# Kernel optimization log

Measured on AMD Instinct MI355X. Metric: run time of the kernel, lower is better.

## Reference

```python
import jax, jax.numpy as jnp
import numpy as np

# PyTorch LSTM gate order: i, f, g, o. Dropout layers are identity in eval mode.

def _lstm_step(w_ih, w_hh, b):
    def step(carry, xt):
        h, c = carry
        g = xt @ w_ih.T + h @ w_hh.T + b
        i, f, gg, o = jnp.split(g, 4, axis=-1)
        c = jax.nn.sigmoid(f) * c + jax.nn.sigmoid(i) * jnp.tanh(gg)
        h = jax.nn.sigmoid(o) * jnp.tanh(c)
        return (h, c), h
    return step


def bilstm(x, wf_ih, wf_hh, bf_ih, bf_hh, wb_ih, wb_hh, bb_ih, bb_hh):
    # x: [B, T, D] -> out: [B, T, 2H]
    B = x.shape[0]
    H = wf_hh.shape[1]
    xt = jnp.swapaxes(x, 0, 1)  # [T, B, D]
    init = (jnp.zeros((B, H), x.dtype), jnp.zeros((B, H), x.dtype))
    _, hf = jax.lax.scan(_lstm_step(wf_ih, wf_hh, bf_ih + bf_hh), init, xt)
    _, hb = jax.lax.scan(_lstm_step(wb_ih, wb_hh, bb_ih + bb_hh), init, xt[::-1])
    hb = hb[::-1]
    return jnp.swapaxes(jnp.concatenate([hf, hb], axis=-1), 0, 1)


def setup_inputs() -> dict:
    key = jax.random.key(0)
    ks = iter(jax.random.split(key, 64))
    d = {"x": jax.random.normal(next(ks), (1024, 1024, 8), jnp.float32)}
    layer_dims = [(16, 20), (40, 20), (40, 10), (20, 10)]
    for li, (din, H) in enumerate(layer_dims, start=1):
        for dr in ("f", "b"):
            d[f"w{li}{dr}_ih"] = 0.1 * jax.random.normal(next(ks), (4 * H, din), jnp.float32)
            d[f"w{li}{dr}_hh"] = 0.1 * jax.random.normal(next(ks), (4 * H, H), jnp.float32)
            d[f"b{li}{dr}_ih"] = 0.1 * jax.random.normal(next(ks), (4 * H,), jnp.float32)
            d[f"b{li}{dr}_hh"] = 0.1 * jax.random.normal(next(ks), (4 * H,), jnp.float32)
    d["fc_w"] = 0.1 * jax.random.normal(next(ks), (1, 20), jnp.float32)
    d["fc_b"] = 0.1 * jax.random.normal(next(ks), (1,), jnp.float32)
    return d


def reference(x,
              w1f_ih, w1f_hh, b1f_ih, b1f_hh, w1b_ih, w1b_hh, b1b_ih, b1b_hh,
              w2f_ih, w2f_hh, b2f_ih, b2f_hh, w2b_ih, w2b_hh, b2b_ih, b2b_hh,
              w3f_ih, w3f_hh, b3f_ih, b3f_hh, w3b_ih, w3b_hh, b3b_ih, b3b_hh,
              w4f_ih, w4f_hh, b4f_ih, b4f_hh, w4b_ih, w4b_hh, b4b_ih, b4b_hh,
              fc_w, fc_b):
    # lag-1 concat: [B,T,8] -> [B,T,16]
    x_lag = jnp.concatenate([jnp.zeros_like(x[:, :1, :]), x[:, :-1, :]], axis=1)
    h = jnp.concatenate([x, x_lag], axis=2)
    h = bilstm(h, w1f_ih, w1f_hh, b1f_ih, b1f_hh, w1b_ih, w1b_hh, b1b_ih, b1b_hh)
    h = bilstm(h, w2f_ih, w2f_hh, b2f_ih, b2f_hh, w2b_ih, w2b_hh, b2b_ih, b2b_hh)
    h = bilstm(h, w3f_ih, w3f_hh, b3f_ih, b3f_hh, w3b_ih, w3b_hh, b3b_ih, b3b_hh)
    h = bilstm(h, w4f_ih, w4f_hh, b4f_ih, b4f_hh, w4b_ih, w4b_hh, b4b_ih, b4b_hh)
    h = h[:, -1, :]  # [B, 20]
    return jax.nn.sigmoid(h @ fc_w.T + fc_b)
```

## Files before the change

### kernel.cpp

```cpp
#include <hip/hip_runtime.h>
#include <hip/hip_fp16.h>
#include <stdint.h>

#define B_TOTAL 1024
#define T_TOTAL 1024
#define LOG2E 1.44269504088896f

typedef _Float16 f16x2 __attribute__((ext_vector_type(2)));

__device__ __forceinline__ float dot2acc(uint32_t xw, f16x2 w, float acc) {
#if __has_builtin(__builtin_amdgcn_fdot2)
    return __builtin_amdgcn_fdot2(__builtin_bit_cast(f16x2, xw), w, acc, false);
#else
    f16x2 xv = __builtin_bit_cast(f16x2, xw);
    return acc + (float)xv.x * (float)w.x + (float)xv.y * (float)w.y;
#endif
}

__device__ __forceinline__ uint32_t packf2(float a, float b) {
    f16x2 t;
    t.x = (_Float16)a;
    t.y = (_Float16)b;
    return __builtin_bit_cast(uint32_t, t);
}

__device__ __forceinline__ float sigm_(float z) {
    float e = __builtin_amdgcn_exp2f(-LOG2E * z);
    return __builtin_amdgcn_rcpf(1.0f + e);
}
__device__ __forceinline__ float tanh_(float z) {
    float e = __builtin_amdgcn_exp2f((2.0f * LOG2E) * z);
    float r = __builtin_amdgcn_rcpf(1.0f + e);
    return __builtin_fmaf(-2.0f, r, 1.0f);
}

__device__ __forceinline__ void wavebar() {
#if __has_builtin(__builtin_amdgcn_wave_barrier)
    __builtin_amdgcn_wave_barrier();
#endif
}

template <int DIN, int H, bool LAYER1, bool STORE_ALL>
__global__ void __launch_bounds__(64, 1) lstm_scan(
    const float* __restrict__ x,
    const __half* __restrict__ inbuf,
    const float* __restrict__ wihf, const float* __restrict__ whhf,
    const float* __restrict__ bihf, const float* __restrict__ bhhf,
    const float* __restrict__ wihb, const float* __restrict__ whhb,
    const float* __restrict__ bihb, const float* __restrict__ bhhb,
    __half* __restrict__ outbuf,
    float* __restrict__ lasth)
{
    constexpr int GPW   = 64 / H;
    constexpr int ND    = DIN / 2;
    constexpr int NH    = H / 2;
    constexpr int HS_DW = (H == 20) ? 12 : 8;

    const int dir  = blockIdx.y;
    const int lane = threadIdx.x;
    const int g    = lane / H;
    const int j    = lane - g * H;
    const int b    = blockIdx.x * GPW + g;
    const bool valid = (g < GPW) && (b < B_TOTAL);
    const int bs   = valid ? b : (B_TOTAL - 1);

    const float* w_ih = dir ? wihb : wihf;
    const float* w_hh = dir ? whhb : whhf;
    const float* b_ih = dir ? bihb : bihf;
    const float* b_hh = dir ? bhhb : bhhf;

    __shared__ uint32_t hsm[GPW + 1][HS_DW];

    f16x2 wih2[4][ND];
    f16x2 whh2[4][NH];
    float bias[4];
#pragma unroll
    for (int q = 0; q < 4; ++q) {
        const int r = q * H + j;
#pragma unroll
        for (int d = 0; d < ND; ++d) {
            f16x2 t;
            t.x = (_Float16)w_ih[r * DIN + 2 * d];
            t.y = (_Float16)w_ih[r * DIN + 2 * d + 1];
            wih2[q][d] = t;
        }
#pragma unroll
        for (int k = 0; k < NH; ++k) {
            f16x2 t;
            t.x = (_Float16)w_hh[r * H + 2 * k];
            t.y = (_Float16)w_hh[r * H + 2 * k + 1];
            whh2[q][k] = t;
        }
        bias[q] = b_ih[r] + b_hh[r];
    }

    const int tstep = dir ? -1 : 1;
    int tt = dir ? (T_TOTAL - 1) : 0;

    __half* op = nullptr;
    ptrdiff_t opstep = 0;
    if constexpr (STORE_ALL) {
        op = outbuf + (size_t)tt * (B_TOTAL * 2 * H) + (size_t)bs * (2 * H) + dir * H + j;
        opstep = (ptrdiff_t)tstep * (B_TOTAL * 2 * H);
    }

    float c = 0.0f;
    float hlast = 0.0f;
    ((__half*)&hsm[g][0])[j] = __float2half(0.0f);
    wavebar();

    auto tail = [&](const uint32_t* hd, float a0, float a1, float a2, float a3) {
#pragma unroll
        for (int k = 0; k < NH; ++k) {
            a0 = dot2acc(hd[k], whh2[0][k], a0);
            a1 = dot2acc(hd[k], whh2[1][k], a1);
            a2 = dot2acc(hd[k], whh2[2][k], a2);
            a3 = dot2acc(hd[k], whh2[3][k], a3);
        }
        const float iv = sigm_(a0);
        const float fv = sigm_(a1);
        const float gv = tanh_(a2);
        const float ov = sigm_(a3);
        c = __builtin_fmaf(fv, c, iv * gv);
        const float h = ov * tanh_(c);
        ((__half*)&hsm[g][0])[j] = __float2half(h);
        wavebar();
        if constexpr (STORE_ALL) {
            if (valid) *op = __float2half(h);
            op += opstep;
        } else {
            hlast = h;
        }
        tt += tstep;
    };

    if constexpr (LAYER1) {
        const float* xrow = x + (size_t)bs * (T_TOTAL * 8);
        uint32_t xcur[4], xlag[4];
        {
            const float4* p = (const float4*)(xrow + (size_t)tt * 8);
            float4 u0 = p[0], u1 = p[1];
            xcur[0] = packf2(u0.x, u0.y); xcur[1] = packf2(u0.z, u0.w);
            xcur[2] = packf2(u1.x, u1.y); xcur[3] = packf2(u1.z, u1.w);
            if (dir) {
                const float4* q = (const float4*)(xrow + (size_t)(tt - 1) * 8);
                float4 v0 = q[0], v1 = q[1];
                xlag[0] = packf2(v0.x, v0.y); xlag[1] = packf2(v0.z, v0.w);
                xlag[2] = packf2(v1.x, v1.y); xlag[3] = packf2(v1.z, v1.w);
            } else {
#pragma unroll
                for (int d = 0; d < 4; ++d) xlag[d] = 0u;
            }
        }

        for (int t = 0; t < T_TOTAL; ++t) {
            uint32_t hd[NH];
#pragma unroll
            for (int k = 0; k < NH; ++k) hd[k] = hsm[g][k];

            float a0 = bias[0], a1 = bias[1], a2 = bias[2], a3 = bias[3];
#pragma unroll
            for (int d = 0; d < 4; ++d) {
                a0 = dot2acc(xcur[d], wih2[0][d], a0);
                a1 = dot2acc(xcur[d], wih2[1][d], a1);
                a2 = dot2acc(xcur[d], wih2[2][d], a2);
                a3 = dot2acc(xcur[d], wih2[3][d], a3);
            }
#pragma unroll
            for (int d = 0; d < 4; ++d) {
                a0 = dot2acc(xlag[d], wih2[0][4 + d], a0);
                a1 = dot2acc(xlag[d], wih2[1][4 + d], a1);
                a2 = dot2acc(xlag[d], wih2[2][4 + d], a2);
                a3 = dot2acc(xlag[d], wih2[3][4 + d], a3);
            }

            const int li = dir ? (tt - 2) : (tt + 1);
            const bool ld = (li >= 0) && (li < T_TOTAL);
            float4 n0 = {0, 0, 0, 0}, n1 = {0, 0, 0, 0};
            if (ld) {
                const float4* p = (const float4*)(xrow + (size_t)li * 8);
                n0 = p[0];
                n1 = p[1];
            }

            tail(hd, a0, a1, a2, a3);

            uint32_t np[4] = {packf2(n0.x, n0.y), packf2(n0.z, n0.w),
                              packf2(n1.x, n1.y), packf2(n1.z, n1.w)};
            if (dir == 0) {
#pragma unroll
                for (int d = 0; d < 4; ++d) { xlag[d] = xcur[d]; xcur[d] = np[d]; }
            } else {
#pragma unroll
                for (int d = 0; d < 4; ++d) {
                    xcur[d] = xlag[d];
                    xlag[d] = ld ? np[d] : 0u;
                }
            }
        }
    } else {
        const ptrdiff_t ipstep = (ptrdiff_t)tstep * (B_TOTAL * ND);
        const uint32_t* ip = (const uint32_t*)inbuf + (size_t)tt * (B_TOTAL * ND) + (size_t)bs * ND;

        uint32_t xb[4][ND];
#pragma unroll
        for (int s = 0; s < 3; ++s) {
#pragma unroll
            for (int d = 0; d < ND; ++d) xb[s][d] = ip[d];
            ip += ipstep;
        }

        auto step = [&](const uint32_t* xc, uint32_t* xn, bool pf) {
            uint32_t hd[NH];
#pragma unroll
            for (int k = 0; k < NH; ++k) hd[k] = hsm[g][k];

            float a0 = bias[0], a1 = bias[1], a2 = bias[2], a3 = bias[3];
#pragma unroll
            for (int d = 0; d < ND; ++d) {
                a0 = dot2acc(xc[d], wih2[0][d], a0);
                a1 = dot2acc(xc[d], wih2[1][d], a1);
                a2 = dot2acc(xc[d], wih2[2][d], a2);
                a3 = dot2acc(xc[d], wih2[3][d], a3);
            }
            if (pf) {
#pragma unroll
                for (int d = 0; d < ND; ++d) xn[d] = ip[d];
                ip += ipstep;
            }
            tail(hd, a0, a1, a2, a3);
        };

        for (int t = 0; t < T_TOTAL; t += 4) {
            step(xb[0], xb[3], t + 3 < T_TOTAL);
            step(xb[1], xb[0], t + 4 < T_TOTAL);
            step(xb[2], xb[1], t + 5 < T_TOTAL);
            step(xb[3], xb[2], t + 6 < T_TOTAL);
        }
    }

    if constexpr (!STORE_ALL) {
        if (valid) lasth[b * H + j] = hlast;
    }
}

__global__ void final_kernel(const __half* __restrict__ l3out,
                             const float* __restrict__ hf4,
                             const float* __restrict__ w_ih,
                             const float* __restrict__ b_ih,
                             const float* __restrict__ b_hh,
                             const float* __restrict__ fc_w,
                             const float* __restrict__ fc_b,
                             float* __restrict__ out)
{
    const int b = blockIdx.x * blockDim.x + threadIdx.x;
    if (b >= B_TOTAL) return;

    float in4[20];
    const __half* p = l3out + (size_t)(T_TOTAL - 1) * (B_TOTAL * 20) + (size_t)b * 20;
#pragma unroll
    for (int i = 0; i < 20; ++i) in4[i] = __half2float(p[i]);

    float z = fc_b[0];
#pragma unroll
    for (int k = 0; k < 10; ++k) z += fc_w[k] * hf4[b * 10 + k];

#pragma unroll
    for (int k = 0; k < 10; ++k) {
        float gi = b_ih[k]      + b_hh[k];
        float gg = b_ih[20 + k] + b_hh[20 + k];
        float go = b_ih[30 + k] + b_hh[30 + k];
#pragma unroll
        for (int i = 0; i < 20; ++i) {
            const float xi = in4[i];
            gi += w_ih[k * 20 + i]        * xi;
            gg += w_ih[(20 + k) * 20 + i] * xi;
            go += w_ih[(30 + k) * 20 + i] * xi;
        }
        const float cc = sigm_(gi) * tanh_(gg);
        const float hb = sigm_(go) * tanh_(cc);
        z += fc_w[10 + k] * hb;
    }
    out[b] = sigm_(z);
}

extern "C" void kernel_launch(void* const* d_in, const int* in_sizes, int n_in,
                              void* d_out, int out_size, void* d_ws, size_t ws_size,
                              hipStream_t stream) {
    const float* x = (const float*)d_in[0];
    auto W = [&](int li, int dr, int k) -> const float* {
        return (const float*)d_in[1 + (li - 1) * 8 + dr * 4 + k];
    };
    const float* fc_w = (const float*)d_in[33];
    const float* fc_b = (const float*)d_in[34];
    float* out = (float*)d_out;

    __half* buf0 = (__half*)d_ws;
    __half* buf1 = buf0 + (size_t)T_TOTAL * B_TOTAL * 40;
    float* hf4 = (float*)(buf1 + (size_t)T_TOTAL * B_TOTAL * 40);

    lstm_scan<16, 20, true, true><<<dim3(342, 2, 1), 64, 0, stream>>>(
        x, nullptr,
        W(1,0,0), W(1,0,1), W(1,0,2), W(1,0,3),
        W(1,1,0), W(1,1,1), W(1,1,2), W(1,1,3),
        buf0, nullptr);

    lstm_scan<40, 20, false, true><<<dim3(342, 2, 1), 64, 0, stream>>>(
        nullptr, buf0,
        W(2,0,0), W(2,0,1), W(2,0,2), W(2,0,3),
        W(2,1,0), W(2,1,1), W(2,1,2), W(2,1,3),
        buf1, nullptr);

    lstm_scan<40, 10, false, true><<<dim3(171, 2, 1), 64, 0, stream>>>(
        nullptr, buf1,
        W(3,0,0), W(3,0,1), W(3,0,2), W(3,0,3),
        W(3,1,0), W(3,1,1), W(3,1,2), W(3,1,3),
        buf0, nullptr);

    lstm_scan<20, 10, false, false><<<dim3(171, 1, 1), 64, 0, stream>>>(
        nullptr, buf0,
        W(4,0,0), W(4,0,1), W(4,0,2), W(4,0,3),
        W(4,0,0), W(4,0,1), W(4,0,2), W(4,0,3),
        nullptr, hf4);

    final_kernel<<<dim3(4, 1, 1), 256, 0, stream>>>(
        buf0, hf4, W(4,1,0), W(4,1,2), W(4,1,3), fc_w, fc_b, out);
}
```

Baseline: 1.731 ms.

## Precompute input-gate projections in a parallel GEMM before each recurrent scan

Each LSTM layer now first runs a fully parallel gates_gemm kernel that computes x·W_ih plus both biases for every timestep and batch row, and stores the gate pre-activations as fp16 pairs in a large workspace buffer. A new lstm_scan2 kernel then reads those precomputed gates and does only the recurrent h·W_hh product and the nonlinearities. This takes the input-projection dot products off the serial per-timestep critical path. The cost is writing and re-reading a gate buffer of several hundred MB per layer, plus an extra fp16 rounding of the gate pre-activations. The original fused path is kept as a fallback when the workspace is too small.

```diff
diff --git a/kernel.cpp b/kernel.cpp
--- a/kernel.cpp
+++ b/kernel.cpp
@@ -38,6 +38,202 @@
 #if __has_builtin(__builtin_amdgcn_wave_barrier)
     __builtin_amdgcn_wave_barrier();
 #endif
+}
+
+template <int D, int H, int NDIR, bool LAYER1>
+__global__ void __launch_bounds__(320) gates_gemm(
+    const float* __restrict__ x,
+    const __half* __restrict__ inact,
+    const float* __restrict__ wf, const float* __restrict__ bfi, const float* __restrict__ bfh,
+    const float* __restrict__ wb, const float* __restrict__ bbi, const float* __restrict__ bbh,
+    uint32_t* __restrict__ gbuf)
+{
+    constexpr int NG  = NDIR * 2 * H;
+    constexpr int YS  = 320 / NG;
+    constexpr int NDW = D / 2;
+
+    const int tid = threadIdx.x;
+    const int c   = tid % NG;
+    const int s   = tid / NG;
+    const int dir = c / (2 * H);
+    const int rem = c % (2 * H);
+    const int j   = rem >> 1;
+    const int p   = rem & 1;
+    const int r0  = p * 2 * H + j;
+    const int r1  = r0 + H;
+
+    const float* w  = (NDIR == 2 && dir) ? wb : wf;
+    const float* bi = (NDIR == 2 && dir) ? bbi : bfi;
+    const float* bh = (NDIR == 2 && dir) ? bbh : bfh;
+
+    f16x2 w0[NDW], w1[NDW];
+#pragma unroll
+    for (int d = 0; d < NDW; ++d) {
+        f16x2 t0, t1;
+        t0.x = (_Float16)w[r0 * D + 2 * d];
+        t0.y = (_Float16)w[r0 * D + 2 * d + 1];
+        t1.x = (_Float16)w[r1 * D + 2 * d];
+        t1.y = (_Float16)w[r1 * D + 2 * d + 1];
+        w0[d] = t0;
+        w1[d] = t1;
+    }
+    const float bias0 = bi[r0] + bh[r0];
+    const float bias1 = bi[r1] + bh[r1];
+
+    const int TB = T_TOTAL * B_TOTAL;
+    for (int tb = blockIdx.x * YS + s; tb < TB; tb += gridDim.x * YS) {
+        uint32_t xr[NDW];
+        if constexpr (LAYER1) {
+            const int t = tb >> 10;
+            const int b = tb & 1023;
+            const float* xp = x + ((size_t)b * T_TOTAL + t) * 8;
+            float4 f0 = ((const float4*)xp)[0];
+            float4 f1 = ((const float4*)xp)[1];
+            float4 l0 = {0, 0, 0, 0}, l1 = {0, 0, 0, 0};
+            if (t > 0) {
+                l0 = ((const float4*)(xp - 8))[0];
+                l1 = ((const float4*)(xp - 8))[1];
+            }
+            xr[0] = packf2(f0.x, f0.y); xr[1] = packf2(f0.z, f0.w);
+            xr[2] = packf2(f1.x, f1.y); xr[3] = packf2(f1.z, f1.w);
+            xr[4] = packf2(l0.x, l0.y); xr[5] = packf2(l0.z, l0.w);
+            xr[6] = packf2(l1.x, l1.y); xr[7] = packf2(l1.z, l1.w);
+        } else {
+            const uint32_t* ip = (const uint32_t*)inact + (size_t)tb * NDW;
+            if constexpr ((NDW % 4) == 0) {
+#pragma unroll
+                for (int q4 = 0; q4 < NDW / 4; ++q4) {
+                    uint4 v = ((const uint4*)ip)[q4];
+                    xr[4 * q4] = v.x; xr[4 * q4 + 1] = v.y;
+                    xr[4 * q4 + 2] = v.z; xr[4 * q4 + 3] = v.w;
+                }
+            } else {
+#pragma unroll
+                for (int q2 = 0; q2 < NDW / 2; ++q2) {
+                    uint2 v = ((const uint2*)ip)[q2];
+                    xr[2 * q2] = v.x; xr[2 * q2 + 1] = v.y;
+                }
+                if constexpr (NDW & 1) xr[NDW - 1] = ip[NDW - 1];
+            }
+        }
+
+        float d0 = bias0, d1 = bias1;
+#pragma unroll
+        for (int d = 0; d < NDW; ++d) {
+            d0 = dot2acc(xr[d], w0[d], d0);
+            d1 = dot2acc(xr[d], w1[d], d1);
+        }
+        gbuf[(size_t)tb * NG + c] = packf2(d0, d1);
+    }
+}
+
+template <int H, int NDIR, bool STORE_ALL>
+__global__ void __launch_bounds__(64, 1) lstm_scan2(
+    const uint32_t* __restrict__ gbuf,
+    const float* __restrict__ whhf, const float* __restrict__ whhb,
+    __half* __restrict__ outact,
+    float* __restrict__ lasth)
+{
+    constexpr int GPW   = 64 / H;
+    constexpr int NH    = H / 2;
+    constexpr int NG    = NDIR * 2 * H;
+    constexpr int HS_DW = (H == 20) ? 12 : 8;
+
+    const int dir  = (NDIR == 2) ? blockIdx.y : 0;
+    const int lane = threadIdx.x;
+    const int g    = lane / H;
+    const int j    = lane - g * H;
+    const int b    = blockIdx.x * GPW + g;
+    const bool valid = (g < GPW) && (b < B_TOTAL);
+    const int bs   = valid ? b : (B_TOTAL - 1);
+
+    const float* w_hh = dir ? whhb : whhf;
+
+    __shared__ uint32_t hsm[GPW + 1][HS_DW];
+
+    f16x2 whh2[4][NH];
+#pragma unroll
+    for (int q = 0; q < 4; ++q) {
+        const int r = q * H + j;
+#pragma unroll
+        for (int k = 0; k < NH; ++k) {
+            f16x2 t;
+            t.x = (_Float16)w_hh[r * H + 2 * k];
+            t.y = (_Float16)w_hh[r * H + 2 * k + 1];
+            whh2[q][k] = t;
+        }
+    }
+
+    const int tstep = dir ? -1 : 1;
+    const int tt0   = dir ? (T_TOTAL - 1) : 0;
+
+    const ptrdiff_t gpstep = (ptrdiff_t)tstep * (B_TOTAL * NG);
+    const uint32_t* gp = gbuf + (size_t)(tt0 * B_TOTAL + bs) * NG + dir * (2 * H) + 2 * j;
+
+    __half* op = nullptr;
+    ptrdiff_t opstep = 0;
+    if constexpr (STORE_ALL) {
+        op = outact + (size_t)(tt0 * B_TOTAL + bs) * (2 * H) + dir * H + j;
+        opstep = (ptrdiff_t)tstep * (B_TOTAL * 2 * H);
+    }
+
+    uint2 qb[4];
+#pragma unroll
+    for (int s = 0; s < 3; ++s) {
+        qb[s] = *(const uint2*)gp;
+        gp += gpstep;
+    }
+
+    float c = 0.0f;
+    float hlast = 0.0f;
+    ((__half*)&hsm[g][0])[j] = __float2half(0.0f);
+    wavebar();
+
+    auto step = [&](const uint2 qc, uint2& qn, bool pf) {
+        uint32_t hd[NH];
+#pragma unroll
+        for (int k = 0; k < NH; ++k) hd[k] = hsm[g][k];
+
+        f16x2 lo = __builtin_bit_cast(f16x2, qc.x);
+        f16x2 hi = __builtin_bit_cast(f16x2, qc.y);
+        float a0 = (float)lo.x, a1 = (float)lo.y;
+        float a2 = (float)hi.x, a3 = (float)hi.y;
+
+        if (pf) { qn = *(const uint2*)gp; gp += gpstep; }
+
+#pragma unroll
+        for (int k = 0; k < NH; ++k) {
+            a0 = dot2acc(hd[k], whh2[0][k], a0);
+            a1 = dot2acc(hd[k], whh2[1][k], a1);
+            a2 = dot2acc(hd[k], whh2[2][k], a2);
+            a3 = dot2acc(hd[k], whh2[3][k], a3);
+        }
+        const float iv = sigm_(a0);
+        const float fv = sigm_(a1);
+        const float gv = tanh_(a2);
+        const float ov = sigm_(a3);
+        c = __builtin_fmaf(fv, c, iv * gv);
+        const float h = ov * tanh_(c);
+        ((__half*)&hsm[g][0])[j] = __float2half(h);
+        wavebar();
+        if constexpr (STORE_ALL) {
+            if (valid) *op = __float2half(h);
+            op += opstep;
+        } else {
+            hlast = h;
+        }
+    };
+
+    for (int t = 0; t < T_TOTAL; t += 4) {
+        step(qb[0], qb[3], t + 3 < T_TOTAL);
+        step(qb[1], qb[0], t + 4 < T_TOTAL);
+        step(qb[2], qb[1], t + 5 < T_TOTAL);
+        step(qb[3], qb[2], t + 6 < T_TOTAL);
+    }
+
+    if constexpr (!STORE_ALL) {
+        if (valid) lasth[b * H + j] = hlast;
+    }
 }
 
 template <int DIN, int H, bool LAYER1, bool STORE_ALL>
@@ -210,7 +406,7 @@
             ip += ipstep;
         }
 
-        auto step = [&](const uint32_t* xc, uint32_t* xn, bool pf) {
+        auto stp = [&](const uint32_t* xc, uint32_t* xn, bool pf) {
             uint32_t hd[NH];
 #pragma unroll
             for (int k = 0; k < NH; ++k) hd[k] = hsm[g][k];
@@ -232,10 +428,10 @@
         };
 
         for (int t = 0; t < T_TOTAL; t += 4) {
-            step(xb[0], xb[3], t + 3 < T_TOTAL);
-            step(xb[1], xb[0], t + 4 < T_TOTAL);
-            step(xb[2], xb[1], t + 5 < T_TOTAL);
-            step(xb[3], xb[2], t + 6 < T_TOTAL);
+            stp(xb[0], xb[3], t + 3 < T_TOTAL);
+            stp(xb[1], xb[0], t + 4 < T_TOTAL);
+            stp(xb[2], xb[1], t + 5 < T_TOTAL);
+            stp(xb[3], xb[2], t + 6 < T_TOTAL);
         }
     }
 
@@ -295,34 +491,72 @@
     const float* fc_b = (const float*)d_in[34];
     float* out = (float*)d_out;
 
-    __half* buf0 = (__half*)d_ws;
-    __half* buf1 = buf0 + (size_t)T_TOTAL * B_TOTAL * 40;
-    float* hf4 = (float*)(buf1 + (size_t)T_TOTAL * B_TOTAL * 40);
-
-    lstm_scan<16, 20, true, true><<<dim3(342, 2, 1), 64, 0, stream>>>(
-        x, nullptr,
-        W(1,0,0), W(1,0,1), W(1,0,2), W(1,0,3),
-        W(1,1,0), W(1,1,1), W(1,1,2), W(1,1,3),
-        buf0, nullptr);
-
-    lstm_scan<40, 20, false, true><<<dim3(342, 2, 1), 64, 0, stream>>>(
-        nullptr, buf0,
-        W(2,0,0), W(2,0,1), W(2,0,2), W(2,0,3),
-        W(2,1,0), W(2,1,1), W(2,1,2), W(2,1,3),
-        buf1, nullptr);
-
-    lstm_scan<40, 10, false, true><<<dim3(171, 2, 1), 64, 0, stream>>>(
-        nullptr, buf1,
-        W(3,0,0), W(3,0,1), W(3,0,2), W(3,0,3),
-        W(3,1,0), W(3,1,1), W(3,1,2), W(3,1,3),
-        buf0, nullptr);
-
-    lstm_scan<20, 10, false, false><<<dim3(171, 1, 1), 64, 0, stream>>>(
-        nullptr, buf0,
-        W(4,0,0), W(4,0,1), W(4,0,2), W(4,0,3),
-        W(4,0,0), W(4,0,1), W(4,0,2), W(4,0,3),
-        nullptr, hf4);
-
-    final_kernel<<<dim3(4, 1, 1), 256, 0, stream>>>(
-        buf0, hf4, W(4,1,0), W(4,1,2), W(4,1,3), fc_w, fc_b, out);
-}
+    const size_t TB = (size_t)T_TOTAL * B_TOTAL;
+    const size_t G_BYTES = TB * 80 * 4;
+    const size_t A_BYTES = TB * 40 * 2;
+    const size_t H4_BYTES = (size_t)B_TOTAL * 10 * 4;
+
+    if (ws_size >= G_BYTES + A_BYTES + H4_BYTES) {
+        uint32_t* G = (uint32_t*)d_ws;
+        __half* A = (__half*)((char*)d_ws + G_BYTES);
+        float* hf4 = (float*)((char*)d_ws + G_BYTES + A_BYTES);
+
+        gates_gemm<16, 20, 2, true><<<2048, 320, 0, stream>>>(
+            x, nullptr,
+            W(1,0,0), W(1,0,2), W(1,0,3),
+            W(1,1,0), W(1,1,2), W(1,1,3), G);
+        lstm_scan2<20, 2, true><<<dim3(342, 2, 1), 64, 0, stream>>>(
+            G, W(1,0,1), W(1,1,1), A, nullptr);
+
+        gates_gemm<40, 20, 2, false><<<2048, 320, 0, stream>>>(
+            nullptr, A,
+            W(2,0,0), W(2,0,2), W(2,0,3),
+            W(2,1,0), W(2,1,2), W(2,1,3), G);
+        lstm_scan2<20, 2, true><<<dim3(342, 2, 1), 64, 0, stream>>>(
+            G, W(2,0,1), W(2,1,1), A, nullptr);
+
+        gates_gemm<40, 10, 2, false><<<2048, 320, 0, stream>>>(
+            nullptr, A,
+            W(3,0,0), W(3,0,2), W(3,0,3),
+            W(3,1,0), W(3,1,2), W(3,1,3), G);
+        lstm_scan2<10, 2, true><<<dim3(171, 2, 1), 64, 0, stream>>>(
+            G, W(3,0,1), W(3,1,1), A, nullptr);
+
+        gates_gemm<20, 10, 1, false><<<2048, 320, 0, stream>>>(
+            nullptr, A,
+            W(4,0,0), W(4,0,2), W(4,0,3),
+            W(4,0,0), W(4,0,2), W(4,0,3), G);
+        lstm_scan2<10, 1, false><<<dim3(171, 1, 1), 64, 0, stream>>>(
+            G, W(4,0,1), W(4,0,1), nullptr, hf4);
+
+        final_kernel<<<dim3(4, 1, 1), 256, 0, stream>>>(
+            A, hf4, W(4,1,0), W(4,1,2), W(4,1,3), fc_w, fc_b, out);
+    } else {
+        __half* buf0 = (__half*)d_ws;
+        __half* buf1 = buf0 + TB * 40;
+        float* hf4 = (float*)(buf1 + TB * 40);
+
+        lstm_scan<16, 20, true, true><<<dim3(342, 2, 1), 64, 0, stream>>>(
+            x, nullptr,
+            W(1,0,0), W(1,0,1), W(1,0,2), W(1,0,3),
+            W(1,1,0), W(1,1,1), W(1,1,2), W(1,1,3),
+            buf0, nullptr);
+        lstm_scan<40, 20, false, true><<<dim3(342, 2, 1), 64, 0, stream>>>(
+            nullptr, buf0,
+            W(2,0,0), W(2,0,1), W(2,0,2), W(2,0,3),
+            W(2,1,0), W(2,1,1), W(2,1,2), W(2,1,3),
+            buf1, nullptr);
+        lstm_scan<40, 10, false, true><<<dim3(171, 2, 1), 64, 0, stream>>>(
+            nullptr, buf1,
+            W(3,0,0), W(3,0,1), W(3,0,2), W(3,0,3),
+            W(3,1,0), W(3,1,1), W(3,1,2), W(3,1,3),
+            buf0, nullptr);
+        lstm_scan<20, 10, false, false><<<dim3(171, 1, 1), 64, 0, stream>>>(
+            nullptr, buf0,
+            W(4,0,0), W(4,0,1), W(4,0,2), W(4,0,3),
+            W(4,0,0), W(4,0,1), W(4,0,2), W(4,0,3),
+            nullptr, hf4);
+        final_kernel<<<dim3(4, 1, 1), 256, 0, stream>>>(
+            buf0, hf4, W(4,1,0), W(4,1,2), W(4,1,3), fc_w, fc_b, out);
+    }
+}
```

Measured after the change: 1.742 ms. Within noise of the previous version (+0.6%).

## Fuse both LSTM directions into one wavefront per batch element with split accumulators

Applied to the files above, without the earlier changes.

Each 64-lane wavefront now handles both forward and backward directions of a single batch element (or two elements for the last layer), replacing the old packing of several batch elements per wave with one direction per grid row. Layer 1 keeps its input weights and inputs in fp32 and uses fma instead of fp16 dot2. The gate dot products are split into two independent accumulator chains to shorten the serial dependency inside each step, and input rows are loaded with vector loads. The launch grows from 684 to 1024 waves and per-wave batch packing drops, which shortens the per-step critical path but uses more waves and leaves idle lanes in layers 3 and 4.

```diff
diff --git a/kernel.cpp b/kernel.cpp
--- a/kernel.cpp
+++ b/kernel.cpp
@@ -40,8 +40,8 @@
 #endif
 }
 
-template <int DIN, int H, bool LAYER1, bool STORE_ALL>
-__global__ void __launch_bounds__(64, 1) lstm_scan(
+template <int DIN, int H, int NDIR, int GPB, bool LAYER1, bool STORE_ALL>
+__global__ void __launch_bounds__(64, 1) lstm_fused(
     const float* __restrict__ x,
     const __half* __restrict__ inbuf,
     const float* __restrict__ wihf, const float* __restrict__ whhf,
@@ -51,184 +51,197 @@
     __half* __restrict__ outbuf,
     float* __restrict__ lasth)
 {
-    constexpr int GPW   = 64 / H;
-    constexpr int ND    = DIN / 2;
-    constexpr int NH    = H / 2;
-    constexpr int HS_DW = (H == 20) ? 12 : 8;
-
-    const int dir  = blockIdx.y;
+    constexpr int LPG = NDIR * H;
+    constexpr int NL  = GPB * LPG;
+    constexpr int ND  = DIN / 2;
+    constexpr int NH  = H / 2;
+    constexpr int NHL = NH / 2;
+    constexpr int HSP = (NH + 3) & ~3;
+
     const int lane = threadIdx.x;
-    const int g    = lane / H;
-    const int j    = lane - g * H;
-    const int b    = blockIdx.x * GPW + g;
-    const bool valid = (g < GPW) && (b < B_TOTAL);
-    const int bs   = valid ? b : (B_TOTAL - 1);
+    const bool act = lane < NL;
+    const int la   = act ? lane : 0;
+    const int g    = la / LPG;
+    const int rr   = la % LPG;
+    const int dir  = (NDIR == 2) ? (rr / H) : 0;
+    const int j    = (NDIR == 2) ? (rr % H) : rr;
+    const int b    = blockIdx.x * GPB + g;
+    const int sgn  = dir ? -1 : 1;
+    int tt         = dir ? (T_TOTAL - 1) : 0;
 
     const float* w_ih = dir ? wihb : wihf;
     const float* w_hh = dir ? whhb : whhf;
     const float* b_ih = dir ? bihb : bihf;
     const float* b_hh = dir ? bhhb : bhhf;
 
-    __shared__ uint32_t hsm[GPW + 1][HS_DW];
-
-    f16x2 wih2[4][ND];
+    __shared__ uint32_t hsm[GPB][NDIR][HSP];
+    uint32_t* hrow = &hsm[g][dir][0];
+    __half*   hhlf = (__half*)hrow;
+
     f16x2 whh2[4][NH];
     float bias[4];
 #pragma unroll
     for (int q = 0; q < 4; ++q) {
-        const int r = q * H + j;
-#pragma unroll
-        for (int d = 0; d < ND; ++d) {
-            f16x2 t;
-            t.x = (_Float16)w_ih[r * DIN + 2 * d];
-            t.y = (_Float16)w_ih[r * DIN + 2 * d + 1];
-            wih2[q][d] = t;
-        }
+        const int r_ = q * H + j;
 #pragma unroll
         for (int k = 0; k < NH; ++k) {
             f16x2 t;
-            t.x = (_Float16)w_hh[r * H + 2 * k];
-            t.y = (_Float16)w_hh[r * H + 2 * k + 1];
+            t.x = (_Float16)w_hh[r_ * H + 2 * k];
+            t.y = (_Float16)w_hh[r_ * H + 2 * k + 1];
             whh2[q][k] = t;
         }
-        bias[q] = b_ih[r] + b_hh[r];
-    }
-
-    const int tstep = dir ? -1 : 1;
-    int tt = dir ? (T_TOTAL - 1) : 0;
+        bias[q] = b_ih[r_] + b_hh[r_];
+    }
+
+    float wih1[LAYER1 ? 64 : 1];
+    f16x2 wih2[LAYER1 ? 1 : 4][LAYER1 ? 1 : ND];
+    if constexpr (LAYER1) {
+#pragma unroll
+        for (int q = 0; q < 4; ++q)
+#pragma unroll
+            for (int i = 0; i < 16; ++i)
+                wih1[q * 16 + i] = w_ih[(q * H + j) * 16 + i];
+    } else {
+#pragma unroll
+        for (int q = 0; q < 4; ++q) {
+            const int r_ = q * H + j;
+#pragma unroll
+            for (int d = 0; d < ND; ++d) {
+                f16x2 t;
+                t.x = (_Float16)w_ih[r_ * DIN + 2 * d];
+                t.y = (_Float16)w_ih[r_ * DIN + 2 * d + 1];
+                wih2[q][d] = t;
+            }
+        }
+    }
 
     __half* op = nullptr;
     ptrdiff_t opstep = 0;
     if constexpr (STORE_ALL) {
-        op = outbuf + (size_t)tt * (B_TOTAL * 2 * H) + (size_t)bs * (2 * H) + dir * H + j;
-        opstep = (ptrdiff_t)tstep * (B_TOTAL * 2 * H);
-    }
-
-    float c = 0.0f;
-    float hlast = 0.0f;
-    ((__half*)&hsm[g][0])[j] = __float2half(0.0f);
+        op = outbuf + ((size_t)tt * B_TOTAL + b) * (2 * H) + dir * H + j;
+        opstep = (ptrdiff_t)sgn * (B_TOTAL * 2 * H);
+    }
+
+    float c = 0.0f, h = 0.0f;
+    if (act) hhlf[j] = __float2half(0.0f);
     wavebar();
 
-    auto tail = [&](const uint32_t* hd, float a0, float a1, float a2, float a3) {
-#pragma unroll
-        for (int k = 0; k < NH; ++k) {
-            a0 = dot2acc(hd[k], whh2[0][k], a0);
-            a1 = dot2acc(hd[k], whh2[1][k], a1);
-            a2 = dot2acc(hd[k], whh2[2][k], a2);
-            a3 = dot2acc(hd[k], whh2[3][k], a3);
-        }
+    auto finish = [&](const float* xl, const float* xh) {
+        uint32_t hd[NH];
+#pragma unroll
+        for (int k = 0; k < NH; ++k) hd[k] = hrow[k];
+        float hl[4] = {0, 0, 0, 0}, hh[4] = {0, 0, 0, 0};
+#pragma unroll
+        for (int k = 0; k < NHL; ++k)
+#pragma unroll
+            for (int q = 0; q < 4; ++q) hl[q] = dot2acc(hd[k], whh2[q][k], hl[q]);
+#pragma unroll
+        for (int k = NHL; k < NH; ++k)
+#pragma unroll
+            for (int q = 0; q < 4; ++q) hh[q] = dot2acc(hd[k], whh2[q][k], hh[q]);
+        const float a0 = (xl[0] + xh[0]) + (hl[0] + hh[0]);
+        const float a1 = (xl[1] + xh[1]) + (hl[1] + hh[1]);
+        const float a2 = (xl[2] + xh[2]) + (hl[2] + hh[2]);
+        const float a3 = (xl[3] + xh[3]) + (hl[3] + hh[3]);
         const float iv = sigm_(a0);
         const float fv = sigm_(a1);
         const float gv = tanh_(a2);
         const float ov = sigm_(a3);
         c = __builtin_fmaf(fv, c, iv * gv);
-        const float h = ov * tanh_(c);
-        ((__half*)&hsm[g][0])[j] = __float2half(h);
+        h = ov * tanh_(c);
+        if (act) hhlf[j] = __float2half(h);
         wavebar();
         if constexpr (STORE_ALL) {
-            if (valid) *op = __float2half(h);
+            if (act) *op = __float2half(h);
             op += opstep;
-        } else {
-            hlast = h;
-        }
-        tt += tstep;
+        }
     };
 
     if constexpr (LAYER1) {
-        const float* xrow = x + (size_t)bs * (T_TOTAL * 8);
-        uint32_t xcur[4], xlag[4];
+        const float* xrow = x + (size_t)b * (T_TOTAL * 8);
+        float xcur[8], xlag[8];
         {
-            const float4* p = (const float4*)(xrow + (size_t)tt * 8);
-            float4 u0 = p[0], u1 = p[1];
-            xcur[0] = packf2(u0.x, u0.y); xcur[1] = packf2(u0.z, u0.w);
-            xcur[2] = packf2(u1.x, u1.y); xcur[3] = packf2(u1.z, u1.w);
-            if (dir) {
-                const float4* q = (const float4*)(xrow + (size_t)(tt - 1) * 8);
-                float4 v0 = q[0], v1 = q[1];
-                xlag[0] = packf2(v0.x, v0.y); xlag[1] = packf2(v0.z, v0.w);
-                xlag[2] = packf2(v1.x, v1.y); xlag[3] = packf2(v1.z, v1.w);
-            } else {
-#pragma unroll
-                for (int d = 0; d < 4; ++d) xlag[d] = 0u;
-            }
-        }
-
+            const float* p = xrow + (size_t)tt * 8;
+#pragma unroll
+            for (int i = 0; i < 8; ++i) xcur[i] = p[i];
+            const float* q = xrow + (size_t)(tt - (dir ? 1 : 0)) * 8;
+#pragma unroll
+            for (int i = 0; i < 8; ++i) xlag[i] = dir ? q[i] : 0.0f;
+        }
         for (int t = 0; t < T_TOTAL; ++t) {
-            uint32_t hd[NH];
-#pragma unroll
-            for (int k = 0; k < NH; ++k) hd[k] = hsm[g][k];
-
-            float a0 = bias[0], a1 = bias[1], a2 = bias[2], a3 = bias[3];
-#pragma unroll
-            for (int d = 0; d < 4; ++d) {
-                a0 = dot2acc(xcur[d], wih2[0][d], a0);
-                a1 = dot2acc(xcur[d], wih2[1][d], a1);
-                a2 = dot2acc(xcur[d], wih2[2][d], a2);
-                a3 = dot2acc(xcur[d], wih2[3][d], a3);
-            }
-#pragma unroll
-            for (int d = 0; d < 4; ++d) {
-                a0 = dot2acc(xlag[d], wih2[0][4 + d], a0);
-                a1 = dot2acc(xlag[d], wih2[1][4 + d], a1);
-                a2 = dot2acc(xlag[d], wih2[2][4 + d], a2);
-                a3 = dot2acc(xlag[d], wih2[3][4 + d], a3);
-            }
-
+            float xl[4], xh[4];
+#pragma unroll
+            for (int q = 0; q < 4; ++q) {
+                float a = bias[q], bsum = 0.0f;
+#pragma unroll
+                for (int i = 0; i < 8; ++i) {
+                    a    = __builtin_fmaf(wih1[q * 16 + i],     xcur[i], a);
+                    bsum = __builtin_fmaf(wih1[q * 16 + 8 + i], xlag[i], bsum);
+                }
+                xl[q] = a; xh[q] = bsum;
+            }
             const int li = dir ? (tt - 2) : (tt + 1);
             const bool ld = (li >= 0) && (li < T_TOTAL);
-            float4 n0 = {0, 0, 0, 0}, n1 = {0, 0, 0, 0};
+            float np[8];
             if (ld) {
-                const float4* p = (const float4*)(xrow + (size_t)li * 8);
-                n0 = p[0];
-                n1 = p[1];
-            }
-
-            tail(hd, a0, a1, a2, a3);
-
-            uint32_t np[4] = {packf2(n0.x, n0.y), packf2(n0.z, n0.w),
-                              packf2(n1.x, n1.y), packf2(n1.z, n1.w)};
-            if (dir == 0) {
-#pragma unroll
-                for (int d = 0; d < 4; ++d) { xlag[d] = xcur[d]; xcur[d] = np[d]; }
+                const float* p = xrow + (size_t)li * 8;
+#pragma unroll
+                for (int i = 0; i < 8; ++i) np[i] = p[i];
             } else {
 #pragma unroll
-                for (int d = 0; d < 4; ++d) {
-                    xcur[d] = xlag[d];
-                    xlag[d] = ld ? np[d] : 0u;
+                for (int i = 0; i < 8; ++i) np[i] = 0.0f;
+            }
+            finish(xl, xh);
+#pragma unroll
+            for (int i = 0; i < 8; ++i) {
+                const float nc = dir ? xlag[i] : np[i];
+                const float nl = dir ? np[i]   : xcur[i];
+                xcur[i] = nc; xlag[i] = nl;
+            }
+            tt += sgn;
+        }
+    } else {
+        const ptrdiff_t ipstep = (ptrdiff_t)sgn * (B_TOTAL * ND);
+        const uint32_t* ip = (const uint32_t*)inbuf + ((size_t)tt * B_TOTAL + b) * ND;
+
+        auto loadrow = [&](uint32_t* dst) {
+            if constexpr ((ND % 4) == 0) {
+#pragma unroll
+                for (int q4 = 0; q4 < ND / 4; ++q4) {
+                    uint4 v = ((const uint4*)ip)[q4];
+                    dst[4 * q4] = v.x; dst[4 * q4 + 1] = v.y;
+                    dst[4 * q4 + 2] = v.z; dst[4 * q4 + 3] = v.w;
                 }
-            }
-        }
-    } else {
-        const ptrdiff_t ipstep = (ptrdiff_t)tstep * (B_TOTAL * ND);
-        const uint32_t* ip = (const uint32_t*)inbuf + (size_t)tt * (B_TOTAL * ND) + (size_t)bs * ND;
+            } else {
+#pragma unroll
+                for (int q2 = 0; q2 < ND / 2; ++q2) {
+                    uint2 v = ((const uint2*)ip)[q2];
+                    dst[2 * q2] = v.x; dst[2 * q2 + 1] = v.y;
+                }
+                if constexpr (ND & 1) dst[ND - 1] = ip[ND - 1];
+            }
+            ip += ipstep;
+        };
 
         uint32_t xb[4][ND];
 #pragma unroll
-        for (int s = 0; s < 3; ++s) {
-#pragma unroll
-            for (int d = 0; d < ND; ++d) xb[s][d] = ip[d];
-            ip += ipstep;
-        }
+        for (int s = 0; s < 3; ++s) loadrow(xb[s]);
 
         auto step = [&](const uint32_t* xc, uint32_t* xn, bool pf) {
-            uint32_t hd[NH];
-#pragma unroll
-            for (int k = 0; k < NH; ++k) hd[k] = hsm[g][k];
-
-            float a0 = bias[0], a1 = bias[1], a2 = bias[2], a3 = bias[3];
-#pragma unroll
-            for (int d = 0; d < ND; ++d) {
-                a0 = dot2acc(xc[d], wih2[0][d], a0);
-                a1 = dot2acc(xc[d], wih2[1][d], a1);
-                a2 = dot2acc(xc[d], wih2[2][d], a2);
-                a3 = dot2acc(xc[d], wih2[3][d], a3);
-            }
-            if (pf) {
-#pragma unroll
-                for (int d = 0; d < ND; ++d) xn[d] = ip[d];
-                ip += ipstep;
-            }
-            tail(hd, a0, a1, a2, a3);
+            float xl[4], xh[4];
+#pragma unroll
+            for (int q = 0; q < 4; ++q) { xl[q] = bias[q]; xh[q] = 0.0f; }
+#pragma unroll
+            for (int d = 0; d < ND / 2; ++d)
+#pragma unroll
+                for (int q = 0; q < 4; ++q) xl[q] = dot2acc(xc[d], wih2[q][d], xl[q]);
+#pragma unroll
+            for (int d = ND / 2; d < ND; ++d)
+#pragma unroll
+                for (int q = 0; q < 4; ++q) xh[q] = dot2acc(xc[d], wih2[q][d], xh[q]);
+            if (pf) loadrow(xn);
+            finish(xl, xh);
+            tt += sgn;
         };
 
         for (int t = 0; t < T_TOTAL; t += 4) {
@@ -240,7 +253,7 @@
     }
 
     if constexpr (!STORE_ALL) {
-        if (valid) lasth[b * H + j] = hlast;
+        if (act) lasth[b * H + j] = h;
     }
 }
 
@@ -295,34 +308,36 @@
     const float* fc_b = (const float*)d_in[34];
     float* out = (float*)d_out;
 
-    __half* buf0 = (__half*)d_ws;
-    __half* buf1 = buf0 + (size_t)T_TOTAL * B_TOTAL * 40;
-    float* hf4 = (float*)(buf1 + (size_t)T_TOTAL * B_TOTAL * 40);
-
-    lstm_scan<16, 20, true, true><<<dim3(342, 2, 1), 64, 0, stream>>>(
+    constexpr size_t MB = 1ull << 20;
+    char* w8 = (char*)d_ws;
+    __half* A0  = (__half*)w8;
+    __half* A1  = (__half*)(w8 + 80 * MB);
+    float*  HF4 = (float*)(w8 + 160 * MB);
+
+    lstm_fused<16, 20, 2, 1, true, true><<<1024, 64, 0, stream>>>(
         x, nullptr,
         W(1,0,0), W(1,0,1), W(1,0,2), W(1,0,3),
         W(1,1,0), W(1,1,1), W(1,1,2), W(1,1,3),
-        buf0, nullptr);
-
-    lstm_scan<40, 20, false, true><<<dim3(342, 2, 1), 64, 0, stream>>>(
-        nullptr, buf0,
+        A0, nullptr);
+
+    lstm_fused<40, 20, 2, 1, false, true><<<1024, 64, 0, stream>>>(
+        nullptr, A0,
         W(2,0,0), W(2,0,1), W(2,0,2), W(2,0,3),
         W(2,1,0), W(2,1,1), W(2,1,2), W(2,1,3),
-        buf1, nullptr);
-
-    lstm_scan<40, 10, false, true><<<dim3(171, 2, 1), 64, 0, stream>>>(
-        nullptr, buf1,
+        A1, nullptr);
+
+    lstm_fused<40, 10, 2, 1, false, true><<<1024, 64, 0, stream>>>(
+        nullptr, A1,
         W(3,0,0), W(3,0,1), W(3,0,2), W(3,0,3),
         W(3,1,0), W(3,1,1), W(3,1,2), W(3,1,3),
-        buf0, nullptr);
-
-    lstm_scan<20, 10, false, false><<<dim3(171, 1, 1), 64, 0, stream>>>(
-        nullptr, buf0,
+        A0, nullptr);
+
+    lstm_fused<20, 10, 1, 2, false, false><<<512, 64, 0, stream>>>(
+        nullptr, A0,
         W(4,0,0), W(4,0,1), W(4,0,2), W(4,0,3),
         W(4,0,0), W(4,0,1), W(4,0,2), W(4,0,3),
-        nullptr, hf4);
+        nullptr, HF4);
 
     final_kernel<<<dim3(4, 1, 1), 256, 0, stream>>>(
-        buf0, hf4, W(4,1,0), W(4,1,2), W(4,1,3), fc_w, fc_b, out);
-}
+        A0, HF4, W(4,1,0), W(4,1,2), W(4,1,3), fc_w, fc_b, out);
+}
```

Result: slower. 2.016 ms (+16.5%).
